# Optimization experiments

Hardware: AMD Instinct MI355X
Metric: run time of the kernel (lower is better)

Reference implementation:

```python
import jax, jax.numpy as jnp
import numpy as np

KEY_DIM = 32
D = 128  # attn_ratio * key_dim
H = 8
DIM = 512
N = 1024
B = 16
EPS = 1e-5


def setup_inputs() -> dict:
    key = jax.random.key(0)
    ks = jax.random.split(key, 5)
    x = jax.random.normal(ks[0], (B, DIM, N), dtype=jnp.float32)
    # grouped Conv1d(dim -> H*(2*key_dim+d), k=1, groups=H): per-group weight [H, 192, 64]
    qkv_w = jax.random.normal(ks[1], (H, 2 * KEY_DIM + D, DIM // H), dtype=jnp.float32) * 0.05
    qkv_b = jax.random.normal(ks[2], (H, 2 * KEY_DIM + D), dtype=jnp.float32) * 0.02
    # proj Conv1d(d*H -> dim, k=1)
    proj_w = jax.random.normal(ks[3], (DIM, D * H), dtype=jnp.float32) * 0.03
    proj_b = jax.random.normal(ks[4], (DIM,), dtype=jnp.float32) * 0.02
    bn_gamma = jnp.ones((DIM,), dtype=jnp.float32)
    bn_beta = jnp.zeros((DIM,), dtype=jnp.float32)
    bn_mean = jnp.zeros((DIM,), dtype=jnp.float32)
    bn_var = jnp.ones((DIM,), dtype=jnp.float32)
    return {"x": x, "qkv_w": qkv_w, "qkv_b": qkv_b, "proj_w": proj_w,
            "proj_b": proj_b, "bn_gamma": bn_gamma, "bn_beta": bn_beta,
            "bn_mean": bn_mean, "bn_var": bn_var}


def reference(x, qkv_w, qkv_b, proj_w, proj_b, bn_gamma, bn_beta, bn_mean, bn_var):
    Bx, C, Nx = x.shape
    scale = KEY_DIM ** (-0.5)
    # grouped 1x1 conv: split channels into H groups of C//H
    xh = x.reshape(Bx, H, C // H, Nx)                      # [B,H,Cg,N]
    qkv = jnp.einsum('bhcn,hoc->bhon', xh, qkv_w) + qkv_b[None, :, :, None]
    q, k, v = jnp.split(qkv, [KEY_DIM, 2 * KEY_DIM], axis=2)  # [B,H,kd,N],[B,H,kd,N],[B,H,d,N]
    # attn[m,n] = sum_c q[c,m]*k[c,n]
    attn = jnp.einsum('bhcm,bhcn->bhmn', q, k) * scale      # [B,H,N,N]
    attn = jax.nn.softmax(attn, axis=-1)
    # out[d,m] = sum_n v[d,n]*attn[m,n]  (v @ attn^T)
    o = jnp.einsum('bhdn,bhmn->bhdm', v, attn)              # [B,H,d,N]
    o = o.reshape(Bx, H * D, Nx)
    # proj: ReLU -> 1x1 conv -> BatchNorm1d (inference mode)
    o = jax.nn.relu(o)
    o = jnp.einsum('bcn,oc->bon', o, proj_w) + proj_b[None, :, None]
    inv = bn_gamma / jnp.sqrt(bn_var + EPS)
    o = o * inv[None, :, None] + (bn_beta - bn_mean * inv)[None, :, None]
    return o
```

## Files before the change

kernel.cpp:

```cpp
#include <hip/hip_runtime.h>
#include <math.h>

typedef unsigned short u16;
typedef unsigned int u32;

#define Bb   16
#define Hh   8
#define KD   32
#define DV   128
#define DIM  512
#define Nn   1024
#define OQKV 192
#define SCALE2 0.25503490221320355f

typedef short bf16x8 __attribute__((ext_vector_type(8)));
typedef float f32x16 __attribute__((ext_vector_type(16)));

#define MFMA32(a, b, c) __builtin_amdgcn_mfma_f32_32x32x16_bf16(a, b, c, 0, 0, 0)

__device__ __forceinline__ float fexp2(float x) {
#if __has_builtin(__builtin_amdgcn_exp2f)
  return __builtin_amdgcn_exp2f(x);
#else
  return exp2f(x);
#endif
}

__device__ __forceinline__ u16 f2bf_rn(float f) {
  return (u16)((__float_as_uint(f) + 0x8000u) >> 16);
}

#if __has_builtin(__builtin_amdgcn_cvt_pk_bf16_f32)
__device__ __forceinline__ u32 pk2(float lo, float hi) {
  auto r = __builtin_amdgcn_cvt_pk_bf16_f32(lo, hi);
  return __builtin_bit_cast(u32, r);
}
#else
__device__ __forceinline__ u32 pk2(float lo, float hi) {
  u32 a = __float_as_uint(lo) + 0x8000u;
  u32 b = __float_as_uint(hi) + 0x8000u;
  return __builtin_amdgcn_perm(b, a, 0x07060302);
}
#endif

#if __has_builtin(__builtin_amdgcn_permlane32_swap)
__device__ __forceinline__ void pswap(u32& a, u32& b) {
  auto r = __builtin_amdgcn_permlane32_swap(a, b, false, false);
  a = r[0]; b = r[1];
}
#else
__device__ __forceinline__ void pswap(u32& a, u32& b) {
  asm("v_permlane32_swap_b32 %0, %1" : "+v"(a), "+v"(b));
}
#endif

__global__ __launch_bounds__(256) void prep_kernel(
    const float* __restrict__ pw, const float* __restrict__ qw,
    const float* __restrict__ pb, const float* __restrict__ g,
    const float* __restrict__ bt, const float* __restrict__ mn,
    const float* __restrict__ vr, u16* __restrict__ Wb,
    u16* __restrict__ Wq, float* __restrict__ invA, float* __restrict__ addB) {
  const int tid = blockIdx.x * 256 + threadIdx.x;
  {
    float4 v = *(const float4*)&pw[(size_t)tid * 4];
    uint2 pk; pk.x = pk2(v.x, v.y); pk.y = pk2(v.z, v.w);
    *(uint2*)&Wb[(size_t)tid * 4] = pk;
  }
  if (tid < 24576) {
    float4 v = *(const float4*)&qw[(size_t)tid * 4];
    uint2 pk; pk.x = pk2(v.x, v.y); pk.y = pk2(v.z, v.w);
    *(uint2*)&Wq[(size_t)tid * 4] = pk;
  }
  if (tid < DIM) {
    float inv = g[tid] * rsqrtf(vr[tid] + 1e-5f);
    invA[tid] = inv;
    addB[tid] = pb[tid] * inv + bt[tid] - mn[tid] * inv;
  }
}

__global__ __launch_bounds__(256) void qkv_kernel(
    const float* __restrict__ x, const u16* __restrict__ Wq,
    const float* __restrict__ bias, u16* __restrict__ Qb,
    u16* __restrict__ Kb, u16* __restrict__ Vb) {
  const int nt = blockIdx.x, bh = blockIdx.y;
  const int b = bh >> 3, h = bh & 7;
  const int tid = threadIdx.x;
  const int wid = tid >> 6, lane = tid & 63;
  const int r32 = lane & 31, hh = lane >> 5;
  const int n0 = nt * 128;

  __shared__ __align__(16) u16 Ws[192 * 72];
  __shared__ __align__(16) u16 Xs[128 * 72];

  const u16* wqp = Wq + (size_t)h * OQKV * 64;
  #pragma unroll
  for (int i = 0; i < 6; ++i) {
    int idx = i * 256 + tid;
    int o = idx >> 3, c8 = (idx & 7) * 8;
    *(uint4*)&Ws[o * 72 + c8] = *(const uint4*)&wqp[o * 64 + c8];
  }
  const float* xp = x + ((size_t)b * DIM + h * 64) * Nn + n0;
  #pragma unroll
  for (int i = 0; i < 4; ++i) {
    int idx = i * 256 + tid;
    int cp = idx >> 5, n4 = (idx & 31) * 4;
    const int c = 2 * cp;
    float4 a = *(const float4*)&xp[(size_t)c * Nn + n4];
    float4 d = *(const float4*)&xp[(size_t)(c + 1) * Nn + n4];
    *(u32*)&Xs[(n4 + 0) * 72 + c] = pk2(a.x, d.x);
    *(u32*)&Xs[(n4 + 1) * 72 + c] = pk2(a.y, d.y);
    *(u32*)&Xs[(n4 + 2) * 72 + c] = pk2(a.z, d.z);
    *(u32*)&Xs[(n4 + 3) * 72 + c] = pk2(a.w, d.w);
  }
  __syncthreads();

  f32x16 acc[6];
  #pragma unroll
  for (int t = 0; t < 6; ++t)
    #pragma unroll
    for (int r = 0; r < 16; ++r) acc[t][r] = 0.0f;

  const int nw = wid * 32;
  #pragma unroll
  for (int k = 0; k < 4; ++k) {
    const int ko = k * 16 + hh * 8;
    bf16x8 xb = *(const bf16x8*)&Xs[(nw + r32) * 72 + ko];
    #pragma unroll
    for (int t = 0; t < 6; ++t) {
      bf16x8 wa = *(const bf16x8*)&Ws[(t * 32 + r32) * 72 + ko];
      acc[t] = MFMA32(wa, xb, acc[t]);
    }
  }

  const int n = n0 + nw + r32;
  const float* bp = bias + h * OQKV;
  #pragma unroll
  for (int t = 0; t < 6; ++t) {
    #pragma unroll
    for (int g = 0; g < 4; ++g) {
      const int ob = t * 32 + 8 * g + 4 * hh;
      float4 bv = *(const float4*)&bp[ob];
      float v0 = acc[t][4 * g + 0] + bv.x;
      float v1 = acc[t][4 * g + 1] + bv.y;
      float v2 = acc[t][4 * g + 2] + bv.z;
      float v3 = acc[t][4 * g + 3] + bv.w;
      if (t == 0) {
        uint2 pk;
        pk.x = pk2(v0 * SCALE2, v1 * SCALE2);
        pk.y = pk2(v2 * SCALE2, v3 * SCALE2);
        *(uint2*)&Qb[((size_t)bh * Nn + n) * 32 + ob] = pk;
      } else if (t == 1) {
        uint2 pk; pk.x = pk2(v0, v1); pk.y = pk2(v2, v3);
        *(uint2*)&Kb[((size_t)bh * Nn + n) * 32 + ob - 32] = pk;
      } else {
        const int d = ob - 64;
        Vb[((size_t)bh * DV + d + 0) * Nn + n] = f2bf_rn(v0);
        Vb[((size_t)bh * DV + d + 1) * Nn + n] = f2bf_rn(v1);
        Vb[((size_t)bh * DV + d + 2) * Nn + n] = f2bf_rn(v2);
        Vb[((size_t)bh * DV + d + 3) * Nn + n] = f2bf_rn(v3);
      }
    }
  }
}

__global__ __launch_bounds__(256) void attn_kernel(
    const u16* __restrict__ Qb, const u16* __restrict__ Kb,
    const u16* __restrict__ Vb, u16* __restrict__ Ot) {
  const int blk = blockIdx.x;
  const int xcd = blk & 7, j = blk >> 3;
  const int bh = (xcd << 4) | (j >> 3);
  const int mt = j & 7;
  const int tid = threadIdx.x;
  const int wid = tid >> 6, lane = tid & 63;
  const int r32 = lane & 31, hh = lane >> 5;
  const int mw = mt * 128 + wid * 32;

  __shared__ __align__(16) u16 Vs[2][128 * 72];

  const u16* qp = Qb + ((size_t)bh * Nn + mw + r32) * 32;
  const bf16x8 qb0 = *(const bf16x8*)&qp[hh * 8];
  const bf16x8 qb1 = *(const bf16x8*)&qp[16 + hh * 8];

  const u16* kbase = Kb + (size_t)bh * Nn * 32;
  const u16* vbase = Vb + (size_t)bh * DV * Nn;

  int sd[4], sn[4];
  #pragma unroll
  for (int i = 0; i < 4; ++i) {
    int idx = i * 256 + tid;
    sd[i] = idx >> 3; sn[i] = (idx & 7) * 8;
  }

  uint4 vreg[4];
  #pragma unroll
  for (int i = 0; i < 4; ++i)
    vreg[i] = *(const uint4*)&vbase[(size_t)sd[i] * Nn + sn[i]];
  #pragma unroll
  for (int i = 0; i < 4; ++i)
    *(uint4*)&Vs[0][sd[i] * 72 + sn[i]] = vreg[i];

  bf16x8 ka[4];
  {
    const u16* kp0 = kbase + (size_t)r32 * 32;
    const u16* kp1 = kbase + (size_t)(32 + r32) * 32;
    ka[0] = *(const bf16x8*)&kp0[hh * 8];
    ka[1] = *(const bf16x8*)&kp0[16 + hh * 8];
    ka[2] = *(const bf16x8*)&kp1[hh * 8];
    ka[3] = *(const bf16x8*)&kp1[16 + hh * 8];
  }
  f32x16 c0, c1;
  #pragma unroll
  for (int r = 0; r < 16; ++r) { c0[r] = 0.0f; c1[r] = 0.0f; }
  c0 = MFMA32(ka[0], qb0, c0);
  c0 = MFMA32(ka[1], qb1, c0);
  c1 = MFMA32(ka[2], qb0, c1);
  c1 = MFMA32(ka[3], qb1, c1);

  {
    const u16* kp0 = kbase + (size_t)(64 + r32) * 32;
    const u16* kp1 = kbase + (size_t)(96 + r32) * 32;
    ka[0] = *(const bf16x8*)&kp0[hh * 8];
    ka[1] = *(const bf16x8*)&kp0[16 + hh * 8];
    ka[2] = *(const bf16x8*)&kp1[hh * 8];
    ka[3] = *(const bf16x8*)&kp1[16 + hh * 8];
  }

  f32x16 o[4];
  #pragma unroll
  for (int t = 0; t < 4; ++t)
    #pragma unroll
    for (int r = 0; r < 16; ++r) o[t][r] = 0.0f;
  float lsum = 0.0f;
  u32 Pk[16];
  union { u32 d[4]; bf16x8 v; } pbf[4];

  auto finishS = [&]() {
    float csum = 0.0f;
    #pragma unroll
    for (int r = 0; r < 16; ++r) { c0[r] = fexp2(c0[r]); csum += c0[r]; }
    #pragma unroll
    for (int r = 0; r < 16; ++r) { c1[r] = fexp2(c1[r]); csum += c1[r]; }
    lsum += csum;
    #pragma unroll
    for (int g = 0; g < 4; ++g) {
      Pk[2 * g]     = pk2(c0[4 * g + 0], c0[4 * g + 1]);
      Pk[2 * g + 1] = pk2(c0[4 * g + 2], c0[4 * g + 3]);
      Pk[8 + 2 * g]     = pk2(c1[4 * g + 0], c1[4 * g + 1]);
      Pk[8 + 2 * g + 1] = pk2(c1[4 * g + 2], c1[4 * g + 3]);
    }
    pswap(Pk[0], Pk[2]);   pswap(Pk[1], Pk[3]);
    pswap(Pk[4], Pk[6]);   pswap(Pk[5], Pk[7]);
    pswap(Pk[8], Pk[10]);  pswap(Pk[9], Pk[11]);
    pswap(Pk[12], Pk[14]); pswap(Pk[13], Pk[15]);
    #pragma unroll
    for (int i = 0; i < 4; ++i) {
      pbf[i].d[0] = Pk[4 * i + 0];
      pbf[i].d[1] = Pk[4 * i + 1];
      pbf[i].d[2] = Pk[4 * i + 2];
      pbf[i].d[3] = Pk[4 * i + 3];
    }
  };

  finishS();

  for (int ch = 0; ch < 15; ++ch) {
    const int p = ch & 1;
    __syncthreads();

    #pragma unroll
    for (int i = 0; i < 4; ++i)
      vreg[i] = *(const uint4*)&vbase[(size_t)sd[i] * Nn + (ch + 1) * 64 + sn[i]];

    __builtin_amdgcn_s_setprio(1);
    #pragma unroll
    for (int r = 0; r < 16; ++r) { c0[r] = 0.0f; c1[r] = 0.0f; }
    c0 = MFMA32(ka[0], qb0, c0);
    c0 = MFMA32(ka[1], qb1, c0);
    c1 = MFMA32(ka[2], qb0, c1);
    c1 = MFMA32(ka[3], qb1, c1);

    bf16x8 kn[4];
    {
      const u16* kp0 = kbase + (size_t)((ch + 2) * 64 + r32) * 32;
      const u16* kp1 = kbase + (size_t)((ch + 2) * 64 + 32 + r32) * 32;
      kn[0] = *(const bf16x8*)&kp0[hh * 8];
      kn[1] = *(const bf16x8*)&kp0[16 + hh * 8];
      kn[2] = *(const bf16x8*)&kp1[hh * 8];
      kn[3] = *(const bf16x8*)&kp1[16 + hh * 8];
    }

    #pragma unroll
    for (int t = 0; t < 4; ++t) {
      const u16* vrow = &Vs[p][(t * 32 + r32) * 72];
      #pragma unroll
      for (int s = 0; s < 4; ++s) {
        bf16x8 va = *(const bf16x8*)&vrow[s * 16 + hh * 8];
        o[t] = MFMA32(va, pbf[s].v, o[t]);
      }
    }
    __builtin_amdgcn_s_setprio(0);

    #pragma unroll
    for (int i = 0; i < 4; ++i)
      *(uint4*)&Vs[1 - p][sd[i] * 72 + sn[i]] = vreg[i];

    finishS();

    #pragma unroll
    for (int i = 0; i < 4; ++i) ka[i] = kn[i];
  }

  __syncthreads();
  __builtin_amdgcn_s_setprio(1);
  #pragma unroll
  for (int t = 0; t < 4; ++t) {
    const u16* vrow = &Vs[1][(t * 32 + r32) * 72];
    #pragma unroll
    for (int s = 0; s < 4; ++s) {
      bf16x8 va = *(const bf16x8*)&vrow[s * 16 + hh * 8];
      o[t] = MFMA32(va, pbf[s].v, o[t]);
    }
  }
  __builtin_amdgcn_s_setprio(0);

  lsum += __shfl_xor(lsum, 32, 64);
  const float inv = 1.0f / lsum;
  const int m = mw + r32;
  const int b = bh >> 3, h = bh & 7;
  u16* obase = Ot + ((size_t)b * Nn + m) * 1024 + h * DV + 4 * hh;
  #pragma unroll
  for (int t = 0; t < 4; ++t) {
    #pragma unroll
    for (int g = 0; g < 4; ++g) {
      float v0 = fmaxf(o[t][4 * g + 0] * inv, 0.0f);
      float v1 = fmaxf(o[t][4 * g + 1] * inv, 0.0f);
      float v2 = fmaxf(o[t][4 * g + 2] * inv, 0.0f);
      float v3 = fmaxf(o[t][4 * g + 3] * inv, 0.0f);
      uint2 pk; pk.x = pk2(v0, v1); pk.y = pk2(v2, v3);
      *(uint2*)&obase[t * 32 + 8 * g] = pk;
    }
  }
}

__global__ __launch_bounds__(256) void proj_kernel(
    const u16* __restrict__ Ot, const u16* __restrict__ Wb,
    const float* __restrict__ invA, const float* __restrict__ addB,
    float* __restrict__ out) {
  const int blk = blockIdx.x;
  const int xcd = blk & 7, rr = blk >> 3;
  const int pairl = rr >> 2, oct = rr & 3;
  const int pair = xcd * 16 + pairl;
  const int b = pair >> 3, nt = pair & 7;
  const int n0 = nt * 128, oc0 = oct * 128;
  const int tid = threadIdx.x;
  const int wid = tid >> 6, lane = tid & 63;
  const int r32 = lane & 31, hh = lane >> 5;
  const int ocw = (wid >> 1) * 64, nw = (wid & 1) * 64;

  __shared__ __align__(16) u16 Ws[128 * 72];
  __shared__ __align__(16) u16 Os[128 * 72];

  f32x16 o[2][2];
  #pragma unroll
  for (int t = 0; t < 2; ++t)
    #pragma unroll
    for (int u = 0; u < 2; ++u)
      #pragma unroll
      for (int r = 0; r < 16; ++r) o[t][u][r] = 0.0f;

  for (int ic0 = 0; ic0 < 1024; ic0 += 64) {
    __syncthreads();
    #pragma unroll
    for (int i = 0; i < 4; ++i) {
      int idx = i * 256 + tid;
      int row = idx >> 3, c8 = (idx & 7) * 8;
      *(uint4*)&Ws[row * 72 + c8] =
          *(const uint4*)&Wb[(size_t)(oc0 + row) * 1024 + ic0 + c8];
    }
    #pragma unroll
    for (int i = 0; i < 4; ++i) {
      int idx = i * 256 + tid;
      int row = idx >> 3, c8 = (idx & 7) * 8;
      *(uint4*)&Os[row * 72 + c8] =
          *(const uint4*)&Ot[((size_t)b * Nn + n0 + row) * 1024 + ic0 + c8];
    }
    __syncthreads();

    #pragma unroll
    for (int s = 0; s < 4; ++s) {
      const int ko = s * 16 + hh * 8;
      bf16x8 a0 = *(const bf16x8*)&Ws[(ocw + r32) * 72 + ko];
      bf16x8 a1 = *(const bf16x8*)&Ws[(ocw + 32 + r32) * 72 + ko];
      bf16x8 b0 = *(const bf16x8*)&Os[(nw + r32) * 72 + ko];
      bf16x8 b1 = *(const bf16x8*)&Os[(nw + 32 + r32) * 72 + ko];
      o[0][0] = MFMA32(a0, b0, o[0][0]);
      o[0][1] = MFMA32(a0, b1, o[0][1]);
      o[1][0] = MFMA32(a1, b0, o[1][0]);
      o[1][1] = MFMA32(a1, b1, o[1][1]);
    }
  }

  #pragma unroll
  for (int t = 0; t < 2; ++t) {
    const int obase = oc0 + ocw + t * 32 + 4 * hh;
    #pragma unroll
    for (int g = 0; g < 4; ++g) {
      const int oc = obase + 8 * g;
      float4 iv = *(const float4*)&invA[oc];
      float4 av = *(const float4*)&addB[oc];
      #pragma unroll
      for (int u = 0; u < 2; ++u) {
        const int n = n0 + nw + u * 32 + r32;
        out[((size_t)b * DIM + oc + 0) * Nn + n] = o[t][u][4 * g + 0] * iv.x + av.x;
        out[((size_t)b * DIM + oc + 1) * Nn + n] = o[t][u][4 * g + 1] * iv.y + av.y;
        out[((size_t)b * DIM + oc + 2) * Nn + n] = o[t][u][4 * g + 2] * iv.z + av.z;
        out[((size_t)b * DIM + oc + 3) * Nn + n] = o[t][u][4 * g + 3] * iv.w + av.w;
      }
    }
  }
}

extern "C" void kernel_launch(void* const* d_in, const int* in_sizes, int n_in,
                              void* d_out, int out_size, void* d_ws,
                              size_t ws_size, hipStream_t stream) {
  const float* x      = (const float*)d_in[0];
  const float* qkv_w  = (const float*)d_in[1];
  const float* qkv_b  = (const float*)d_in[2];
  const float* proj_w = (const float*)d_in[3];
  const float* proj_b = (const float*)d_in[4];
  const float* bn_g   = (const float*)d_in[5];
  const float* bn_b   = (const float*)d_in[6];
  const float* bn_m   = (const float*)d_in[7];
  const float* bn_v   = (const float*)d_in[8];
  float* out = (float*)d_out;

  char* ws = (char*)d_ws;
  u16* Qb   = (u16*)(ws);
  u16* Kb   = (u16*)(ws + 8388608);
  u16* Vb   = (u16*)(ws + 16777216);
  u16* Ot   = (u16*)(ws + 50331648);
  u16* Wb   = (u16*)(ws + 83886080);
  u16* Wq   = (u16*)(ws + 84934656);
  float* invA = (float*)(ws + 85131264);
  float* addB = (float*)(ws + 85133312);

  prep_kernel<<<dim3(512), 256, 0, stream>>>(
      proj_w, qkv_w, proj_b, bn_g, bn_b, bn_m, bn_v, Wb, Wq, invA, addB);
  qkv_kernel<<<dim3(8, Bb * Hh), 256, 0, stream>>>(x, Wq, qkv_b, Qb, Kb, Vb);
  attn_kernel<<<dim3(1024), 256, 0, stream>>>(Qb, Kb, Vb, Ot);
  proj_kernel<<<dim3(512), 256, 0, stream>>>(Ot, Wb, invA, addB, out);
}
```

Before: 188.3 us.

## Software-pipeline proj GEMM with double-buffered LDS and register prefetch

The projection kernel now uses two LDS buffers and keeps two chunks of weights and activations in registers, loaded ahead of use. Global loads for later K-chunks are issued while MFMAs run on the current chunk. This replaces the two barriers per iteration with one, and raises wave priority around the MFMA block. The cost is more LDS and registers, and the final iterations prefetch past the end of the K range. Those extra reads go out of bounds and their data is never used.

After: 250.4 us. 33.0% more time.

```diff
diff --git a/kernel.cpp b/kernel.cpp
--- a/kernel.cpp
+++ b/kernel.cpp
@@ -357,8 +357,17 @@
   const int r32 = lane & 31, hh = lane >> 5;
   const int ocw = (wid >> 1) * 64, nw = (wid & 1) * 64;
 
-  __shared__ __align__(16) u16 Ws[128 * 72];
-  __shared__ __align__(16) u16 Os[128 * 72];
+  __shared__ __align__(16) u16 Ws[2][128 * 72];
+  __shared__ __align__(16) u16 Os[2][128 * 72];
+
+  int srow[4], sc8[4];
+  #pragma unroll
+  for (int i = 0; i < 4; ++i) {
+    int idx = i * 256 + tid;
+    srow[i] = idx >> 3; sc8[i] = (idx & 7) * 8;
+  }
+  const u16* wsrc = Wb + (size_t)oc0 * 1024;
+  const u16* osrc = Ot + ((size_t)b * Nn + n0) * 1024;
 
   f32x16 o[2][2];
   #pragma unroll
@@ -368,37 +377,63 @@
       #pragma unroll
       for (int r = 0; r < 16; ++r) o[t][u][r] = 0.0f;
 
-  for (int ic0 = 0; ic0 < 1024; ic0 += 64) {
-    __syncthreads();
-    #pragma unroll
-    for (int i = 0; i < 4; ++i) {
-      int idx = i * 256 + tid;
-      int row = idx >> 3, c8 = (idx & 7) * 8;
-      *(uint4*)&Ws[row * 72 + c8] =
-          *(const uint4*)&Wb[(size_t)(oc0 + row) * 1024 + ic0 + c8];
-    }
-    #pragma unroll
-    for (int i = 0; i < 4; ++i) {
-      int idx = i * 256 + tid;
-      int row = idx >> 3, c8 = (idx & 7) * 8;
-      *(uint4*)&Os[row * 72 + c8] =
-          *(const uint4*)&Ot[((size_t)b * Nn + n0 + row) * 1024 + ic0 + c8];
-    }
-    __syncthreads();
-
-    #pragma unroll
-    for (int s = 0; s < 4; ++s) {
-      const int ko = s * 16 + hh * 8;
-      bf16x8 a0 = *(const bf16x8*)&Ws[(ocw + r32) * 72 + ko];
-      bf16x8 a1 = *(const bf16x8*)&Ws[(ocw + 32 + r32) * 72 + ko];
-      bf16x8 b0 = *(const bf16x8*)&Os[(nw + r32) * 72 + ko];
-      bf16x8 b1 = *(const bf16x8*)&Os[(nw + 32 + r32) * 72 + ko];
-      o[0][0] = MFMA32(a0, b0, o[0][0]);
-      o[0][1] = MFMA32(a0, b1, o[0][1]);
-      o[1][0] = MFMA32(a1, b0, o[1][0]);
-      o[1][1] = MFMA32(a1, b1, o[1][1]);
-    }
-  }
+  uint4 wA[4], oA[4], wB[4], oB[4];
+  #pragma unroll
+  for (int i = 0; i < 4; ++i) {
+    wA[i] = *(const uint4*)&wsrc[(size_t)srow[i] * 1024 + sc8[i]];
+    oA[i] = *(const uint4*)&osrc[(size_t)srow[i] * 1024 + sc8[i]];
+  }
+  #pragma unroll
+  for (int i = 0; i < 4; ++i) {
+    *(uint4*)&Ws[0][srow[i] * 72 + sc8[i]] = wA[i];
+    *(uint4*)&Os[0][srow[i] * 72 + sc8[i]] = oA[i];
+  }
+  #pragma unroll
+  for (int i = 0; i < 4; ++i) {
+    wA[i] = *(const uint4*)&wsrc[(size_t)srow[i] * 1024 + 128 + sc8[i]];
+    oA[i] = *(const uint4*)&osrc[(size_t)srow[i] * 1024 + 128 + sc8[i]];
+    wB[i] = *(const uint4*)&wsrc[(size_t)srow[i] * 1024 + 64 + sc8[i]];
+    oB[i] = *(const uint4*)&osrc[(size_t)srow[i] * 1024 + 64 + sc8[i]];
+  }
+
+#define PROJ_STEP(CHUNK, RBUF, WSET, OSET)                                     \
+  {                                                                            \
+    __syncthreads();                                                           \
+    _Pragma("unroll")                                                          \
+    for (int i = 0; i < 4; ++i) {                                              \
+      *(uint4*)&Ws[RBUF ^ 1][srow[i] * 72 + sc8[i]] = WSET[i];                 \
+      *(uint4*)&Os[RBUF ^ 1][srow[i] * 72 + sc8[i]] = OSET[i];                 \
+    }                                                                          \
+    {                                                                          \
+      const size_t ic = (size_t)((CHUNK) + 3) * 64;                            \
+      _Pragma("unroll")                                                        \
+      for (int i = 0; i < 4; ++i) {                                            \
+        WSET[i] = *(const uint4*)&wsrc[(size_t)srow[i] * 1024 + ic + sc8[i]];  \
+        OSET[i] = *(const uint4*)&osrc[(size_t)srow[i] * 1024 + ic + sc8[i]];  \
+      }                                                                        \
+    }                                                                          \
+    __builtin_amdgcn_s_setprio(1);                                             \
+    _Pragma("unroll")                                                          \
+    for (int s = 0; s < 4; ++s) {                                              \
+      const int ko = s * 16 + hh * 8;                                          \
+      bf16x8 a0 = *(const bf16x8*)&Ws[RBUF][(ocw + r32) * 72 + ko];            \
+      bf16x8 a1 = *(const bf16x8*)&Ws[RBUF][(ocw + 32 + r32) * 72 + ko];       \
+      bf16x8 b0 = *(const bf16x8*)&Os[RBUF][(nw + r32) * 72 + ko];             \
+      bf16x8 b1 = *(const bf16x8*)&Os[RBUF][(nw + 32 + r32) * 72 + ko];        \
+      o[0][0] = MFMA32(a0, b0, o[0][0]);                                       \
+      o[0][1] = MFMA32(a0, b1, o[0][1]);                                       \
+      o[1][0] = MFMA32(a1, b0, o[1][0]);                                       \
+      o[1][1] = MFMA32(a1, b1, o[1][1]);                                       \
+    }                                                                          \
+    __builtin_amdgcn_s_setprio(0);                                             \
+  }
+
+  for (int pr = 0; pr < 8; ++pr) {
+    const int ch = 2 * pr;
+    PROJ_STEP(ch, 0, wB, oB);
+    PROJ_STEP(ch + 1, 1, wA, oA);
+  }
+#undef PROJ_STEP
 
   #pragma unroll
   for (int t = 0; t < 2; ++t) {
```
